# Kernel tuning notes

Measured on AMD Instinct MI355X. Metric: run time of the kernel, lower is better.

## Reference

```python
import jax, jax.numpy as jnp
import numpy as np

N, D, DC, L, K, H = 131072, 12, 4, 4, 8, 64
S = D // 2          # coupling split
B = 3.0             # spline interval [-B, B]
SLOPE = 0.2         # LeakyReLU negative slope
TOUT = (3 * K - 1) * S


def setup_inputs() -> dict:
    key = jax.random.key(0)
    ks = iter(jax.random.split(key, 40))
    def nrm(shape, scale):
        return jax.random.normal(next(ks), shape, jnp.float32) * scale
    x = jax.random.normal(next(ks), (N, D), jnp.float32)
    x_cond = jax.random.normal(next(ks), (N, DC), jnp.float32)
    rng = np.random.default_rng(0)
    convP = jnp.asarray(np.stack([np.eye(D, dtype=np.float32)[rng.permutation(D)] for _ in range(L)]))
    convS = jnp.asarray((rng.uniform(0.5, 1.5, (L, D)) * rng.choice([-1.0, 1.0], (L, D))).astype(np.float32))
    inp = {"x": x, "x_cond": x_cond, "convP": convP, "convS": convS,
           "convL": nrm((L, D, D), 0.1), "convU": nrm((L, D, D), 0.1)}
    for name, nin in (("net1", S), ("net2", S), ("nc1", DC), ("nc2", DC)):
        inp[name + "_W0"] = nrm((L, nin, H), 0.3)
        inp[name + "_b0"] = nrm((L, H), 0.05)
        inp[name + "_Wh"] = nrm((L, 2, H, H), 0.15)
        inp[name + "_bh"] = nrm((L, 2, H), 0.05)
        inp[name + "_Wl"] = nrm((L, H, TOUT), 0.15)
        inp[name + "_bl"] = nrm((L, TOUT), 0.05)
    return inp


def _leaky(h):
    return jnp.where(h >= 0, h, SLOPE * h)


def _mlp(h, W0, b0, Wh, bh, Wl, bl):
    # Linear->LeakyReLU x n_layers (LeakyReLU also after the last Linear, as in torch MLP)
    h = _leaky(h @ W0 + b0)
    for i in range(Wh.shape[0]):
        h = _leaky(h @ Wh[i] + bh[i])
    return _leaky(h @ Wl + bl)


def _spline_params(thetas):
    th = thetas.reshape(-1, S, 3 * K - 1)
    w = jax.nn.softmax(th[..., :K], axis=-1) * 2 * B
    hgt = jax.nn.softmax(th[..., K:2 * K], axis=-1) * 2 * B
    d = jax.nn.softplus(th[..., 2 * K:])
    d = jnp.pad(d, ((0, 0), (0, 0), (1, 1)), constant_values=1.0)   # [N,S,K+1]
    return w, hgt, d


def _rqs(X, widths, heights, derivs):
    # X [N,S]; widths/heights [N,S,K]; derivs [N,S,K+1]
    pad = jnp.full(X.shape + (1,), -B, X.dtype)
    # last boundary gets +1e-6 inside find_bin (in-place in torch) before search AND gathers
    bx = jnp.concatenate([pad, jnp.cumsum(widths, -1) - B], -1).at[..., -1].set(B + 1e-6)
    by = jnp.concatenate([pad, jnp.cumsum(heights, -1) - B], -1).at[..., -1].set(B)
    Xc = jnp.clip(X, -B, B)   # outside-interval values are overwritten below
    k = jnp.clip(jnp.sum(Xc[..., None] >= bx, -1) - 1, 0, K - 1)
    def g(a, idx):
        return jnp.take_along_axis(a, idx[..., None], -1)[..., 0]
    xk, xk1 = g(bx, k), g(bx, k + 1)
    yk, yk1 = g(by, k), g(by, k + 1)
    dk, dk1 = g(derivs, k), g(derivs, k + 1)
    s = (yk1 - yk) / (xk1 - xk)
    xi = (Xc - xk) / (xk1 - xk)
    den = s + (dk1 + dk - 2 * s) * xi * (1 - xi)
    Y = yk + (yk1 - yk) * (s * xi ** 2 + dk * xi * (1 - xi)) / den
    dydx = s ** 2 * (dk1 * xi ** 2 + 2 * s * xi * (1 - xi) + dk * (1 - xi) ** 2) / den ** 2
    inside = (X <= B) & (X >= -B)
    Y = jnp.where(inside, Y, X)
    ld = jnp.where(inside, jnp.log(dydx), 0.0)
    return Y, jnp.sum(ld, -1)


def reference(x, x_cond, convP, convS, convL, convU,
              net1_W0, net1_b0, net1_Wh, net1_bh, net1_Wl, net1_bl,
              net2_W0, net2_b0, net2_Wh, net2_bh, net2_Wl, net2_bl,
              nc1_W0, nc1_b0, nc1_Wh, nc1_bh, nc1_Wl, nc1_bl,
              nc2_W0, nc2_b0, nc2_Wh, nc2_bh, nc2_Wl, nc2_bl):
    logdet = jnp.zeros(x.shape[0], x.dtype)
    eye = jnp.eye(D, dtype=x.dtype)
    for l in range(L):
        # GLOW 1x1 conv (LU-parameterized)
        W = convP[l] @ (jnp.tril(convL[l], -1) + eye) @ (jnp.triu(convU[l], 1) + jnp.diag(convS[l]))
        x = x @ W
        logdet = logdet + jnp.sum(jnp.log(jnp.abs(convS[l])))
        # NSF_CL2 coupling
        first, second = x[:, S:], x[:, :S]
        t = _mlp(x_cond, nc1_W0[l], nc1_b0[l], nc1_Wh[l], nc1_bh[l], nc1_Wl[l], nc1_bl[l]) * \
            _mlp(second, net1_W0[l], net1_b0[l], net1_Wh[l], net1_bh[l], net1_Wl[l], net1_bl[l])
        w, hgt, d = _spline_params(t)
        first, ld = _rqs(first, w, hgt, d)
        logdet = logdet + ld
        t = _mlp(x_cond, nc2_W0[l], nc2_b0[l], nc2_Wh[l], nc2_bh[l], nc2_Wl[l], nc2_bl[l]) * \
            _mlp(first, net2_W0[l], net2_b0[l], net2_Wh[l], net2_bh[l], net2_Wl[l], net2_bl[l])
        w, hgt, d = _spline_params(t)
        second, ld = _rqs(second, w, hgt, d)
        logdet = logdet + ld
        x = jnp.concatenate([second, first], axis=-1)
    prior_logprob = jnp.sum(-0.5 * x ** 2 - 0.5 * float(np.log(2 * np.pi)), axis=-1)
    return (x, logdet, prior_logprob)
```

## Files before the change

### kernel.cpp

```cpp
#include <hip/hip_runtime.h>
#include <math.h>

typedef _Float16 f16;
typedef _Float16 f16x8 __attribute__((ext_vector_type(8)));
typedef __fp16 h2 __attribute__((ext_vector_type(2)));
typedef float f32x4 __attribute__((ext_vector_type(4)));
typedef unsigned int uint32;
typedef unsigned short ushort16;

#define NSAMP 131072
#define DD 12
#define LLAYERS 4
#define KK 8
#define BV 3.0f
#define BLK 256
#define NLW 17920
#define WS_WH 512
#define WS_WL 8704
#define THROW 152
#define XROW 16
#define SENTD 0.54132485f

__device__ __forceinline__ uint32 packh(float a, float b){
    union { f16 h; ushort16 u; } x, y;
    x.h = (f16)a; y.h = (f16)b;
    return (uint32)x.u | ((uint32)y.u << 16);
}
__device__ __forceinline__ float unpl(uint32 v){ union { ushort16 u; f16 h; } c; c.u = (ushort16)v; return (float)c.h; }
__device__ __forceinline__ float unph(uint32 v){ union { ushort16 u; f16 h; } c; c.u = (ushort16)(v >> 16); return (float)c.h; }

__device__ __forceinline__ h2 u2h(uint32 x){ union { uint32 u; h2 h; } c; c.u = x; return c.h; }
__device__ __forceinline__ uint32 h2u(h2 x){ union { h2 h; uint32 u; } c; c.h = x; return c.u; }
__device__ __forceinline__ h2 lk2(h2 x){
    h2 k = { (__fp16)0.2f, (__fp16)0.2f };
    return __builtin_elementwise_max(x, x * k);
}
__device__ __forceinline__ h2 pkrtz(float a, float b){ return __builtin_amdgcn_cvt_pkrtz(a, b); }
__device__ __forceinline__ float frcp(float x){ return __builtin_amdgcn_rcpf(x); }

__device__ __forceinline__ f32x4 MF(f16x8 a, f16x8 b, f32x4 c){
    return __builtin_amdgcn_mfma_f32_16x16x32_f16(a, b, c, 0, 0, 0);
}

__device__ __forceinline__ const f16x8* actRd(const f16* actW, int s, int fb){
    return (const f16x8*)((const char*)actW + s * 128 + (fb ^ ((s & 7) << 4)));
}
__device__ __forceinline__ uint2* actWr(f16* actW, int s, int fb){
    return (uint2*)((char*)actW + s * 128 + (fb ^ ((s & 7) << 4)));
}

extern "C" __global__ void nsflow_prep(
        const float* __restrict__ n1W0, const float* __restrict__ n1Wh, const float* __restrict__ n1Wl,
        const float* __restrict__ n1b0, const float* __restrict__ n1bh, const float* __restrict__ n1bl,
        const float* __restrict__ n2W0, const float* __restrict__ n2Wh, const float* __restrict__ n2Wl,
        const float* __restrict__ n2b0, const float* __restrict__ n2bh, const float* __restrict__ n2bl,
        const float* __restrict__ c1W0, const float* __restrict__ c1Wh, const float* __restrict__ c1Wl,
        const float* __restrict__ c1b0, const float* __restrict__ c1bh, const float* __restrict__ c1bl,
        const float* __restrict__ c2W0, const float* __restrict__ c2Wh, const float* __restrict__ c2Wl,
        const float* __restrict__ c2b0, const float* __restrict__ c2bh, const float* __restrict__ c2bl,
        const float* __restrict__ convP, const float* __restrict__ convS,
        const float* __restrict__ convL, const float* __restrict__ convU,
        f16* __restrict__ ws_hi, f16* __restrict__ ws_lo,
        uint32* __restrict__ wsbc, uint32* __restrict__ wsbh, float* __restrict__ wsWc){
    int NL = blockIdx.y;
    int off = blockIdx.x * 256 + threadIdx.x;
    int layer = NL >> 2, net = NL & 3;

    const float *W0, *Wh, *Wl, *b0, *bh; int nin;
    if (net == 0){ W0 = c1W0; Wh = c1Wh; Wl = c1Wl; b0 = c1b0; bh = c1bh; nin = 4; }
    else if (net == 1){ W0 = n1W0; Wh = n1Wh; Wl = n1Wl; b0 = n1b0; bh = n1bh; nin = 6; }
    else if (net == 2){ W0 = c2W0; Wh = c2Wh; Wl = c2Wl; b0 = c2b0; bh = c2bh; nin = 4; }
    else { W0 = n2W0; Wh = n2Wh; Wl = n2Wl; b0 = n2b0; bh = n2bh; nin = 6; }

    if (off < 17920){
        float w = 0.f;
        if (off < 512){
            int mt = off >> 7, r = off & 127, ln = r >> 3, j = r & 7;
            int row = mt * 16 + ln;
            if (j < nin) w = W0[(layer * nin + j) * 64 + row];
            else if (j == 7) w = b0[layer * 64 + row];
        } else if (off < 8704){
            int o = off - 512; int h = o >> 12; o &= 4095;
            int t = o >> 9, ln = (o >> 3) & 63, j = o & 7;
            int mt = t >> 1, ks = t & 1;
            int k = ks * 32 + (ln >> 4) * 8 + j, row = mt * 16 + (ln & 15);
            w = Wh[((layer * 2 + h) * 64 + k) * 64 + row];
        } else {
            int o = off - 8704;
            int t = o >> 9, ln = (o >> 3) & 63, j = o & 7;
            int mt = t >> 1, ks = t & 1;
            int k = ks * 32 + (ln >> 4) * 8 + j, m = mt * 16 + (ln & 15);
            int dd = m / 24, p = m - dd * 24;
            if (p < 23) w = Wl[(layer * 64 + k) * 138 + dd * 23 + p];
        }
        f16 hi = (f16)w;
        f16 lo = (f16)(w - (float)hi);
        ws_hi[NL * NLW + off] = hi;
        ws_lo[NL * NLW + off] = lo;
    } else if (off < 18064){
        int mm = off - 17920;
        if (net == 0 || net == 2){
            int halfI = net >> 1;
            int s = layer * 2 + halfI;
            bool isn = mm >= 72;
            int m0 = 2 * (isn ? mm - 72 : mm);
            const float* bb = isn ? (halfI ? n2bl : n1bl) : (halfI ? c2bl : c1bl);
            int dd0 = m0 / 24, p0 = m0 - dd0 * 24;
            int m1 = m0 + 1;
            int dd1 = m1 / 24, p1 = m1 - dd1 * 24;
            float v0 = (p0 < 23) ? bb[layer * 138 + dd0 * 23 + p0] : 0.f;
            float v1 = (p1 < 23) ? bb[layer * 138 + dd1 * 23 + p1] : 0.f;
            wsbc[s * 144 + mm] = packh(v0, v1);
        }
    } else if (off < 18128){
        int q = off - 18064;
        int h = q >> 5, r = q & 31, m0 = 2 * r;
        wsbh[NL * 64 + q] = packh(bh[(layer * 2 + h) * 64 + m0], bh[(layer * 2 + h) * 64 + m0 + 1]);
    } else if (off < 18705 && NL == 0){
        int idx = off - 18128;
        if (idx < 576){
            int l = idx / 144, r = idx - l * 144;
            int i = r / 12, j = r - i * 12;
            const float* P = convP + l * 144;
            const float* Lm = convL + l * 144;
            const float* Um = convU + l * 144;
            const float* Sv = convS + l * 12;
            float acc = 0.f;
            for (int a = 0; a < 12; ++a){
                float inner = 0.f;
                for (int bb2 = 0; bb2 < 12; ++bb2){
                    float m1 = (bb2 < a) ? Lm[a * 12 + bb2] : (bb2 == a ? 1.f : 0.f);
                    float m2 = (j > bb2) ? Um[bb2 * 12 + j] : (j == bb2 ? Sv[j] : 0.f);
                    inner = fmaf(m1, m2, inner);
                }
                acc = fmaf(P[i * 12 + a], inner, acc);
            }
            wsWc[idx] = acc;
        } else if (idx == 576){
            float sacc = 0.f;
            for (int q2 = 0; q2 < LLAYERS * 12; ++q2) sacc += __logf(fabsf(convS[q2]));
            wsWc[576] = sacc;
        }
    }
}

__device__ __forceinline__ void gemmL0c(const f16* __restrict__ ah, const f16* __restrict__ al,
                                        int xc0, int xc1, f16* actW, int lane){
    int l15 = lane & 15, g = lane >> 4;
    f16x8 Z = {};
    f16x8 Bf[4];
#pragma unroll
    for (int nt = 0; nt < 4; ++nt){
        union { uint4 u; f16x8 v; } cc;
        cc.u.x = (uint32)__shfl(xc0, nt * 16 + l15, 64);
        cc.u.y = (uint32)__shfl(xc1, nt * 16 + l15, 64);
        cc.u.z = 0u;
        cc.u.w = 0x3C000000u;
        Bf[nt] = cc.v;
    }
    bool g0 = (g == 0);
#pragma unroll
    for (int mt = 0; mt < 4; ++mt){
        f16x8 Ah = g0 ? *(const f16x8*)(ah + (mt * 16 + l15) * 8) : Z;
        f16x8 Al = g0 ? *(const f16x8*)(al + (mt * 16 + l15) * 8) : Z;
#pragma unroll
        for (int nt = 0; nt < 4; ++nt){
            f32x4 acc = {0.f, 0.f, 0.f, 0.f};
            acc = MF(Ah, Bf[nt], acc);
            acc = MF(Al, Bf[nt], acc);
            uint2 v = { h2u(lk2(pkrtz(acc[0], acc[1]))), h2u(lk2(pkrtz(acc[2], acc[3]))) };
            *actWr(actW, nt * 16 + l15, mt * 32 + g * 8) = v;
        }
    }
}

__device__ __forceinline__ void gemmL0n(const f16* __restrict__ ah, const f16* __restrict__ al,
                                        const f16* src, int offE,
                                        f16* actW, int lane, int widS){
    int l15 = lane & 15, g = lane >> 4;
    f16x8 Z = {};
    f16x8 Bf[4];
#pragma unroll
    for (int nt = 0; nt < 4; ++nt)
        Bf[nt] = *(const f16x8*)(src + (widS + nt * 16 + l15) * XROW + offE);
    bool g0 = (g == 0);
#pragma unroll
    for (int mt = 0; mt < 4; ++mt){
        f16x8 Ah = g0 ? *(const f16x8*)(ah + (mt * 16 + l15) * 8) : Z;
        f16x8 Al = g0 ? *(const f16x8*)(al + (mt * 16 + l15) * 8) : Z;
#pragma unroll
        for (int nt = 0; nt < 4; ++nt){
            f32x4 acc = {0.f, 0.f, 0.f, 0.f};
            acc = MF(Ah, Bf[nt], acc);
            acc = MF(Al, Bf[nt], acc);
            uint2 v = { h2u(lk2(pkrtz(acc[0], acc[1]))), h2u(lk2(pkrtz(acc[2], acc[3]))) };
            *actWr(actW, nt * 16 + l15, mt * 32 + g * 8) = v;
        }
    }
}

__device__ __forceinline__ void gemm64(const f16* __restrict__ ah,
                                       const uint32* __restrict__ bq,
                                       f16* actW, int lane){
    int l15 = lane & 15, g = lane >> 4;
    f16x8 Bf[4][2];
#pragma unroll
    for (int nt = 0; nt < 4; ++nt)
#pragma unroll
        for (int ks = 0; ks < 2; ++ks)
            Bf[nt][ks] = *actRd(actW, nt * 16 + l15, ks * 64 + g * 16);
#pragma unroll
    for (int mt = 0; mt < 4; ++mt){
        f16x8 Ah0 = *(const f16x8*)(ah + ((mt * 2 + 0) * 64 + lane) * 8);
        f16x8 Ah1 = *(const f16x8*)(ah + ((mt * 2 + 1) * 64 + lane) * 8);
        uint2 bp = *(const uint2*)(bq + mt * 8 + g * 2);
#pragma unroll
        for (int nt = 0; nt < 4; ++nt){
            f32x4 acc = {0.f, 0.f, 0.f, 0.f};
            acc = MF(Ah0, Bf[nt][0], acc);
            acc = MF(Ah1, Bf[nt][1], acc);
            uint2 v = { h2u(lk2(pkrtz(acc[0], acc[1]) + u2h(bp.x))),
                        h2u(lk2(pkrtz(acc[2], acc[3]) + u2h(bp.y))) };
            *actWr(actW, nt * 16 + l15, mt * 32 + g * 8) = v;
        }
    }
}

__device__ __forceinline__ float spline_pair(const f16* thW, f16* xst,
                                             int sbase, int halfI, int lane){
    float vsum = 0.f;
    int s32 = lane & 31;
    int hi5 = lane >> 5;
#pragma unroll 1
    for (int pass = 0; pass < 3; ++pass){
        int dd = pass * 2 + hi5;

        const f16* tr = thW + s32 * THROW + dd * 24;
        f16x8 t0 = *(const f16x8*)(tr);
        f16x8 t1 = *(const f16x8*)(tr + 8);
        f16x8 t2 = *(const f16x8*)(tr + 16);
        float th[23];
#pragma unroll
        for (int j = 0; j < 8; ++j) th[j] = (float)t0[j];
#pragma unroll
        for (int j = 0; j < 8; ++j) th[8 + j] = (float)t1[j];
#pragma unroll
        for (int j = 0; j < 7; ++j) th[16 + j] = (float)t2[j];

        float mw = th[0];
#pragma unroll
        for (int j = 1; j < KK; ++j) mw = fmaxf(mw, th[j]);
        float ew[KK]; float swsum = 0.f;
#pragma unroll
        for (int j = 0; j < KK; ++j){ ew[j] = __expf(th[j] - mw); swsum += ew[j]; }
        float iw_ = 6.0f * frcp(swsum);
        float mh = th[KK];
#pragma unroll
        for (int j = 1; j < KK; ++j) mh = fmaxf(mh, th[KK + j]);
        float eh[KK]; float shsum = 0.f;
#pragma unroll
        for (int j = 0; j < KK; ++j){ eh[j] = __expf(th[KK + j] - mh); shsum += eh[j]; }
        float ih_ = 6.0f * frcp(shsum);

        int sidx = sbase + s32;
        int slot = halfI ? dd : 8 + dd;
        float X = (float)xst[sidx * XROW + slot];
        float Xc = fminf(fmaxf(X, -BV), BV);

        float cx = -BV, cy = -BV;
        float xk = -BV, xk1 = BV, yk = -BV, yk1 = BV;
        float tl = SENTD, trh = SENTD;
#pragma unroll
        for (int j = 0; j < KK; ++j){
            float nx = (j == KK - 1) ? (BV + 1e-6f) : (cx + ew[j] * iw_);
            float ny = (j == KK - 1) ? BV : (cy + eh[j] * ih_);
            bool sel = (j == 0) || (Xc >= cx);
            if (sel){
                xk = cx; xk1 = nx; yk = cy; yk1 = ny;
                tl = (j == 0) ? SENTD : th[15 + j];
                trh = (j == KK - 1) ? SENTD : th[16 + j];
            }
            cx = nx; cy = ny;
        }
        float dk, dk1;
        {
            float z = __expf(-fabsf(tl));
            dk = fmaxf(tl, 0.f) + __logf(1.0f + z);
            float z2 = __expf(-fabsf(trh));
            dk1 = fmaxf(trh, 0.f) + __logf(1.0f + z2);
        }
        float idx_ = frcp(xk1 - xk);
        float s_ = (yk1 - yk) * idx_;
        float xi = (Xc - xk) * idx_;
        float om = 1.0f - xi;
        float xo = xi * om;
        float den = s_ + (dk1 + dk - 2.0f * s_) * xo;
        float invden = frcp(den);
        float Y = yk + (yk1 - yk) * (s_ * xi * xi + dk * xo) * invden;
        float dydx = s_ * s_ * (dk1 * xi * xi + 2.0f * s_ * xo + dk * om * om) * invden * invden;
        bool inside = (X <= BV) && (X >= -BV);
        float Yo = inside ? Y : X;
        float ldv = inside ? __logf(dydx) : 0.f;
        xst[sidx * XROW + slot] = (f16)Yo;
        vsum += ldv;
    }
    vsum += __shfl_xor(vsum, 32, 64);
    return vsum;
}

#define TAILP(NT0, NT1, BC0A, BC0B, BC1A, BC1B)                                        \
{                                                                                      \
    f16x8 Bn0a = *actRd(actW, NT0 * 16 + l15, g * 16);                                 \
    f16x8 Bn0b = *actRd(actW, NT0 * 16 + l15, 64 + g * 16);                            \
    f16x8 Bn1a = *actRd(actW, NT1 * 16 + l15, g * 16);                                 \
    f16x8 Bn1b = *actRd(actW, NT1 * 16 + l15, 64 + g * 16);                            \
    _Pragma("unroll")                                                                  \
    for (int mt = 0; mt < 9; ++mt){                                                    \
        const f16* pch = whC + WS_WL + (mt * 128 + lane) * 8;                          \
        const f16* pnh = whN + WS_WL + (mt * 128 + lane) * 8;                          \
        f16x8 AhC0 = *(const f16x8*)(pch);                                             \
        f16x8 AhC1 = *(const f16x8*)(pch + 512);                                       \
        f16x8 AhN0 = *(const f16x8*)(pnh);                                             \
        f16x8 AhN1 = *(const f16x8*)(pnh + 512);                                       \
        uint2 cq = *(const uint2*)(bcn + mt * 8 + g * 2);                              \
        uint2 nq = *(const uint2*)(bcn + 72 + mt * 8 + g * 2);                         \
        f32x4 ac = {0.f,0.f,0.f,0.f}, an = {0.f,0.f,0.f,0.f};                          \
        ac = MF(AhC0, BC0A, ac); ac = MF(AhC1, BC0B, ac);                              \
        an = MF(AhN0, Bn0a, an); an = MF(AhN1, Bn0b, an);                              \
        h2 c01 = lk2(pkrtz(ac[0], ac[1]) + u2h(cq.x));                                 \
        h2 c23 = lk2(pkrtz(ac[2], ac[3]) + u2h(cq.y));                                 \
        h2 n01 = lk2(pkrtz(an[0], an[1]) + u2h(nq.x));                                 \
        h2 n23 = lk2(pkrtz(an[2], an[3]) + u2h(nq.y));                                 \
        uint2 tv0 = { h2u(c01 * n01), h2u(c23 * n23) };                                \
        *(uint2*)(thW + l15 * THROW + mt * 16 + g4) = tv0;                             \
        f32x4 ac2 = {0.f,0.f,0.f,0.f}, an2 = {0.f,0.f,0.f,0.f};                        \
        ac2 = MF(AhC0, BC1A, ac2); ac2 = MF(AhC1, BC1B, ac2);                          \
        an2 = MF(AhN0, Bn1a, an2); an2 = MF(AhN1, Bn1b, an2);                          \
        h2 d01 = lk2(pkrtz(ac2[0], ac2[1]) + u2h(cq.x));                               \
        h2 d23 = lk2(pkrtz(ac2[2], ac2[3]) + u2h(cq.y));                               \
        h2 m01 = lk2(pkrtz(an2[0], an2[1]) + u2h(nq.x));                               \
        h2 m23 = lk2(pkrtz(an2[2], an2[3]) + u2h(nq.y));                               \
        uint2 tv1 = { h2u(d01 * m01), h2u(d23 * m23) };                                \
        *(uint2*)(thW + (16 + l15) * THROW + mt * 16 + g4) = tv1;                      \
    }                                                                                  \
    { float v = spline_pair(thW, xstS, widS + NT0 * 16, halfI, lane);                  \
      if ((lane >> 5) == (NT0 >> 1)) logdet += v; }                                    \
}

extern "C" __global__ void __launch_bounds__(BLK, 2)
nsflow_main(const float* __restrict__ x_in, const float* __restrict__ xc_in,
            const f16* __restrict__ wsh, const f16* __restrict__ wsl,
            const uint32* __restrict__ wsbc, const uint32* __restrict__ wsbh,
            const float* __restrict__ wsWc,
            float* __restrict__ out){
    __shared__ f16 xstS[256 * XROW];
    __shared__ f16 actS[4 * 64 * 64];
    __shared__ f16 thS[4 * 32 * THROW];

    int tid0 = threadIdx.x;
    int lane = tid0 & 63, wid = tid0 >> 6, widS = wid * 64;
    int l15 = lane & 15, g = lane >> 4, g4 = g * 4;
    int gsamp = blockIdx.x * BLK + tid0;

    float xr[DD];
    int xc0, xc1;
    {
        const float4* xv = (const float4*)(x_in + (size_t)gsamp * DD);
        float4 a0 = xv[0], a1 = xv[1], a2 = xv[2];
        xr[0]=a0.x; xr[1]=a0.y; xr[2]=a0.z; xr[3]=a0.w;
        xr[4]=a1.x; xr[5]=a1.y; xr[6]=a1.z; xr[7]=a1.w;
        xr[8]=a2.x; xr[9]=a2.y; xr[10]=a2.z; xr[11]=a2.w;
        float4 c0 = *(const float4*)(xc_in + (size_t)gsamp * 4);
        xc0 = (int)packh(c0.x, c0.y);
        xc1 = (int)packh(c0.z, c0.w);
    }

    float logdet = wsWc[576];
    f16* actW = actS + wid * 4096;
    f16* thW = thS + wid * (32 * THROW);

#pragma unroll 1
    for (int l = 0; l < LLAYERS; ++l){
        if (l > 0){
            uint4 r0 = *(const uint4*)(xstS + tid0 * XROW);
            uint4 r1 = *(const uint4*)(xstS + tid0 * XROW + 8);
            xr[0]=unpl(r0.x); xr[1]=unph(r0.x); xr[2]=unpl(r0.y); xr[3]=unph(r0.y);
            xr[4]=unpl(r0.z); xr[5]=unph(r0.z);
            xr[6]=unpl(r1.x); xr[7]=unph(r1.x); xr[8]=unpl(r1.y); xr[9]=unph(r1.y);
            xr[10]=unpl(r1.z); xr[11]=unph(r1.z);
        }
        float xn[DD];
#pragma unroll
        for (int j = 0; j < DD; ++j) xn[j] = 0.f;
#pragma unroll
        for (int i = 0; i < DD; ++i){
            const float4* wr = (const float4*)(wsWc + l * 144 + i * 12);
            float4 w0 = wr[0], w1 = wr[1], w2 = wr[2];
            float xi = xr[i];
            xn[0]=fmaf(xi,w0.x,xn[0]); xn[1]=fmaf(xi,w0.y,xn[1]); xn[2]=fmaf(xi,w0.z,xn[2]); xn[3]=fmaf(xi,w0.w,xn[3]);
            xn[4]=fmaf(xi,w1.x,xn[4]); xn[5]=fmaf(xi,w1.y,xn[5]); xn[6]=fmaf(xi,w1.z,xn[6]); xn[7]=fmaf(xi,w1.w,xn[7]);
            xn[8]=fmaf(xi,w2.x,xn[8]); xn[9]=fmaf(xi,w2.y,xn[9]); xn[10]=fmaf(xi,w2.z,xn[10]); xn[11]=fmaf(xi,w2.w,xn[11]);
        }
#pragma unroll
        for (int j = 0; j < DD; ++j) xr[j] = xn[j];
        {
            uint4 s0 = { packh(xr[0],xr[1]), packh(xr[2],xr[3]), packh(xr[4],xr[5]), 0x3C000000u };
            uint4 s1 = { packh(xr[6],xr[7]), packh(xr[8],xr[9]), packh(xr[10],xr[11]), 0x3C000000u };
            *(uint4*)(xstS + tid0 * XROW) = s0;
            *(uint4*)(xstS + tid0 * XROW + 8) = s1;
        }

#pragma unroll 1
        for (int halfI = 0; halfI < 2; ++halfI){
            const f16* whC = wsh + (size_t)(l * 4 + halfI * 2) * NLW;
            const f16* wlC = wsl + (size_t)(l * 4 + halfI * 2) * NLW;
            const f16* whN = whC + NLW;
            const f16* wlN = wlC + NLW;
            const uint32* bhC = wsbh + (l * 4 + halfI * 2) * 64;
            const uint32* bhN = bhC + 64;
            const uint32* bcn = wsbc + (l * 2 + halfI) * 144;

            gemmL0c(whC, wlC, xc0, xc1, actW, lane);
            gemm64(whC + WS_WH, bhC, actW, lane);
            gemm64(whC + WS_WH + 4096, bhC + 32, actW, lane);
            f16x8 Bc0a = *actRd(actW,      l15, g * 16);
            f16x8 Bc0b = *actRd(actW,      l15, 64 + g * 16);
            f16x8 Bc1a = *actRd(actW, 16 + l15, g * 16);
            f16x8 Bc1b = *actRd(actW, 16 + l15, 64 + g * 16);
            f16x8 Bc2a = *actRd(actW, 32 + l15, g * 16);
            f16x8 Bc2b = *actRd(actW, 32 + l15, 64 + g * 16);
            f16x8 Bc3a = *actRd(actW, 48 + l15, g * 16);
            f16x8 Bc3b = *actRd(actW, 48 + l15, 64 + g * 16);

            gemmL0n(whN, wlN, xstS, halfI * 8, actW, lane, widS);
            gemm64(whN + WS_WH, bhN, actW, lane);
            gemm64(whN + WS_WH + 4096, bhN + 32, actW, lane);

            TAILP(0, 1, Bc0a, Bc0b, Bc1a, Bc1b)
            TAILP(2, 3, Bc2a, Bc2b, Bc3a, Bc3b)
        }
    }

    {
        uint4 r0 = *(const uint4*)(xstS + tid0 * XROW);
        uint4 r1 = *(const uint4*)(xstS + tid0 * XROW + 8);
        xr[0]=unpl(r0.x); xr[1]=unph(r0.x); xr[2]=unpl(r0.y); xr[3]=unph(r0.y);
        xr[4]=unpl(r0.z); xr[5]=unph(r0.z);
        xr[6]=unpl(r1.x); xr[7]=unph(r1.x); xr[8]=unpl(r1.y); xr[9]=unph(r1.y);
        xr[10]=unpl(r1.z); xr[11]=unph(r1.z);
    }
    float pr = 0.f;
#pragma unroll
    for (int j = 0; j < DD; ++j) pr = fmaf(-0.5f * xr[j], xr[j], pr);
    pr -= DD * 0.91893853320467274f;

    float4* ov = (float4*)(out + (size_t)gsamp * DD);
    ov[0] = make_float4(xr[0], xr[1], xr[2], xr[3]);
    ov[1] = make_float4(xr[4], xr[5], xr[6], xr[7]);
    ov[2] = make_float4(xr[8], xr[9], xr[10], xr[11]);
    out[(size_t)NSAMP * DD + gsamp] = logdet;
    out[(size_t)NSAMP * DD + NSAMP + gsamp] = pr;
}

extern "C" void kernel_launch(void* const* d_in, const int* in_sizes, int n_in,
                              void* d_out, int out_size, void* d_ws, size_t ws_size,
                              hipStream_t stream) {
    (void)in_sizes; (void)n_in; (void)out_size; (void)ws_size;
    const float* a[30];
    for (int i = 0; i < 30; ++i) a[i] = (const float*)d_in[i];
    f16* wsh = (f16*)d_ws;
    f16* wsl = wsh + 16 * NLW;
    uint32* wsbc = (uint32*)(wsl + 16 * NLW);
    uint32* wsbh = wsbc + 8 * 144;
    float* wsWc  = (float*)(wsbh + 16 * 64);

    dim3 pg(74, 16);
    nsflow_prep<<<pg, 256, 0, stream>>>(
        a[6], a[8], a[10], a[7], a[9], a[11],
        a[12], a[14], a[16], a[13], a[15], a[17],
        a[18], a[20], a[22], a[19], a[21], a[23],
        a[24], a[26], a[28], a[25], a[27], a[29],
        a[2], a[3], a[4], a[5],
        wsh, wsl, wsbc, wsbh, wsWc);

    nsflow_main<<<NSAMP / BLK, BLK, 0, stream>>>(
        a[0], a[1], wsh, wsl, wsbc, wsbh, wsWc, (float*)d_out);
}
```

Baseline: 191.8 us.

## Shrink blocks to one wave and process spline tail in 16-sample chunks

Blocks go from four waves of 256 samples to a single 64-sample wave, with shared buffers sized per wave, and launch bounds raised to ask for three blocks per CU. The final projection and spline stage now runs in four 16-sample chunks instead of two 32-sample chunks. That shrinks the theta staging buffer and the live registers in the tail, aiming at higher occupancy. In exchange the spline loop leaves half the lanes idle on its second pass, and more small blocks must be scheduled.

```diff
diff --git a/kernel.cpp b/kernel.cpp
--- a/kernel.cpp
+++ b/kernel.cpp
@@ -13,7 +13,7 @@
 #define LLAYERS 4
 #define KK 8
 #define BV 3.0f
-#define BLK 256
+#define BLK 64
 #define NLW 17920
 #define WS_WH 512
 #define WS_WL 8704
@@ -176,13 +176,13 @@
 
 __device__ __forceinline__ void gemmL0n(const f16* __restrict__ ah, const f16* __restrict__ al,
                                         const f16* src, int offE,
-                                        f16* actW, int lane, int widS){
+                                        f16* actW, int lane){
     int l15 = lane & 15, g = lane >> 4;
     f16x8 Z = {};
     f16x8 Bf[4];
 #pragma unroll
     for (int nt = 0; nt < 4; ++nt)
-        Bf[nt] = *(const f16x8*)(src + (widS + nt * 16 + l15) * XROW + offE);
+        Bf[nt] = *(const f16x8*)(src + (nt * 16 + l15) * XROW + offE);
     bool g0 = (g == 0);
 #pragma unroll
     for (int mt = 0; mt < 4; ++mt){
@@ -226,16 +226,16 @@
     }
 }
 
-__device__ __forceinline__ float spline_pair(const f16* thW, f16* xst,
-                                             int sbase, int halfI, int lane){
+__device__ __forceinline__ float spline_chunk(const f16* thW, f16* xst,
+                                              int sbase, int halfI, int lane){
     float vsum = 0.f;
-    int s32 = lane & 31;
-    int hi5 = lane >> 5;
 #pragma unroll 1
-    for (int pass = 0; pass < 3; ++pass){
-        int dd = pass * 2 + hi5;
-
-        const f16* tr = thW + s32 * THROW + dd * 24;
+    for (int pass = 0; pass < 2; ++pass){
+        if (pass == 1 && lane >= 32) break;
+        int dd = pass * 4 + (lane >> 4);
+        int s16 = lane & 15;
+
+        const f16* tr = thW + s16 * THROW + dd * 24;
         f16x8 t0 = *(const f16x8*)(tr);
         f16x8 t1 = *(const f16x8*)(tr + 8);
         f16x8 t2 = *(const f16x8*)(tr + 16);
@@ -262,7 +262,7 @@
         for (int j = 0; j < KK; ++j){ eh[j] = __expf(th[KK + j] - mh); shsum += eh[j]; }
         float ih_ = 6.0f * frcp(shsum);
 
-        int sidx = sbase + s32;
+        int sidx = sbase + s16;
         int slot = halfI ? dd : 8 + dd;
         float X = (float)xst[sidx * XROW + slot];
         float Xc = fminf(fmaxf(X, -BV), BV);
@@ -304,16 +304,15 @@
         xst[sidx * XROW + slot] = (f16)Yo;
         vsum += ldv;
     }
+    vsum += __shfl_xor(vsum, 16, 64);
     vsum += __shfl_xor(vsum, 32, 64);
     return vsum;
 }
 
-#define TAILP(NT0, NT1, BC0A, BC0B, BC1A, BC1B)                                        \
+#define TAILP(NT, BCA, BCB)                                                            \
 {                                                                                      \
-    f16x8 Bn0a = *actRd(actW, NT0 * 16 + l15, g * 16);                                 \
-    f16x8 Bn0b = *actRd(actW, NT0 * 16 + l15, 64 + g * 16);                            \
-    f16x8 Bn1a = *actRd(actW, NT1 * 16 + l15, g * 16);                                 \
-    f16x8 Bn1b = *actRd(actW, NT1 * 16 + l15, 64 + g * 16);                            \
+    f16x8 Bna = *actRd(actW, NT * 16 + l15, g * 16);                                   \
+    f16x8 Bnb = *actRd(actW, NT * 16 + l15, 64 + g * 16);                              \
     _Pragma("unroll")                                                                  \
     for (int mt = 0; mt < 9; ++mt){                                                    \
         const f16* pch = whC + WS_WL + (mt * 128 + lane) * 8;                          \
@@ -325,42 +324,32 @@
         uint2 cq = *(const uint2*)(bcn + mt * 8 + g * 2);                              \
         uint2 nq = *(const uint2*)(bcn + 72 + mt * 8 + g * 2);                         \
         f32x4 ac = {0.f,0.f,0.f,0.f}, an = {0.f,0.f,0.f,0.f};                          \
-        ac = MF(AhC0, BC0A, ac); ac = MF(AhC1, BC0B, ac);                              \
-        an = MF(AhN0, Bn0a, an); an = MF(AhN1, Bn0b, an);                              \
+        ac = MF(AhC0, BCA, ac); ac = MF(AhC1, BCB, ac);                                \
+        an = MF(AhN0, Bna, an); an = MF(AhN1, Bnb, an);                                \
         h2 c01 = lk2(pkrtz(ac[0], ac[1]) + u2h(cq.x));                                 \
         h2 c23 = lk2(pkrtz(ac[2], ac[3]) + u2h(cq.y));                                 \
         h2 n01 = lk2(pkrtz(an[0], an[1]) + u2h(nq.x));                                 \
         h2 n23 = lk2(pkrtz(an[2], an[3]) + u2h(nq.y));                                 \
         uint2 tv0 = { h2u(c01 * n01), h2u(c23 * n23) };                                \
         *(uint2*)(thW + l15 * THROW + mt * 16 + g4) = tv0;                             \
-        f32x4 ac2 = {0.f,0.f,0.f,0.f}, an2 = {0.f,0.f,0.f,0.f};                        \
-        ac2 = MF(AhC0, BC1A, ac2); ac2 = MF(AhC1, BC1B, ac2);                          \
-        an2 = MF(AhN0, Bn1a, an2); an2 = MF(AhN1, Bn1b, an2);                          \
-        h2 d01 = lk2(pkrtz(ac2[0], ac2[1]) + u2h(cq.x));                               \
-        h2 d23 = lk2(pkrtz(ac2[2], ac2[3]) + u2h(cq.y));                               \
-        h2 m01 = lk2(pkrtz(an2[0], an2[1]) + u2h(nq.x));                               \
-        h2 m23 = lk2(pkrtz(an2[2], an2[3]) + u2h(nq.y));                               \
-        uint2 tv1 = { h2u(d01 * m01), h2u(d23 * m23) };                                \
-        *(uint2*)(thW + (16 + l15) * THROW + mt * 16 + g4) = tv1;                      \
     }                                                                                  \
-    { float v = spline_pair(thW, xstS, widS + NT0 * 16, halfI, lane);                  \
-      if ((lane >> 5) == (NT0 >> 1)) logdet += v; }                                    \
-}
-
-extern "C" __global__ void __launch_bounds__(BLK, 2)
+    { float v = spline_chunk(thW, xstS, NT * 16, halfI, lane);                         \
+      if (g == NT) logdet += v; }                                                      \
+}
+
+extern "C" __global__ void __launch_bounds__(BLK, 3)
 nsflow_main(const float* __restrict__ x_in, const float* __restrict__ xc_in,
             const f16* __restrict__ wsh, const f16* __restrict__ wsl,
             const uint32* __restrict__ wsbc, const uint32* __restrict__ wsbh,
             const float* __restrict__ wsWc,
             float* __restrict__ out){
-    __shared__ f16 xstS[256 * XROW];
-    __shared__ f16 actS[4 * 64 * 64];
-    __shared__ f16 thS[4 * 32 * THROW];
-
-    int tid0 = threadIdx.x;
-    int lane = tid0 & 63, wid = tid0 >> 6, widS = wid * 64;
+    __shared__ f16 xstS[BLK * XROW];
+    __shared__ f16 actS[64 * 64];
+    __shared__ f16 thS[16 * THROW];
+
+    int lane = threadIdx.x & 63;
     int l15 = lane & 15, g = lane >> 4, g4 = g * 4;
-    int gsamp = blockIdx.x * BLK + tid0;
+    int gsamp = blockIdx.x * BLK + lane;
 
     float xr[DD];
     int xc0, xc1;
@@ -376,14 +365,14 @@
     }
 
     float logdet = wsWc[576];
-    f16* actW = actS + wid * 4096;
-    f16* thW = thS + wid * (32 * THROW);
+    f16* actW = actS;
+    f16* thW = thS;
 
 #pragma unroll 1
     for (int l = 0; l < LLAYERS; ++l){
         if (l > 0){
-            uint4 r0 = *(const uint4*)(xstS + tid0 * XROW);
-            uint4 r1 = *(const uint4*)(xstS + tid0 * XROW + 8);
+            uint4 r0 = *(const uint4*)(xstS + lane * XROW);
+            uint4 r1 = *(const uint4*)(xstS + lane * XROW + 8);
             xr[0]=unpl(r0.x); xr[1]=unph(r0.x); xr[2]=unpl(r0.y); xr[3]=unph(r0.y);
             xr[4]=unpl(r0.z); xr[5]=unph(r0.z);
             xr[6]=unpl(r1.x); xr[7]=unph(r1.x); xr[8]=unpl(r1.y); xr[9]=unph(r1.y);
@@ -406,8 +395,8 @@
         {
             uint4 s0 = { packh(xr[0],xr[1]), packh(xr[2],xr[3]), packh(xr[4],xr[5]), 0x3C000000u };
             uint4 s1 = { packh(xr[6],xr[7]), packh(xr[8],xr[9]), packh(xr[10],xr[11]), 0x3C000000u };
-            *(uint4*)(xstS + tid0 * XROW) = s0;
-            *(uint4*)(xstS + tid0 * XROW + 8) = s1;
+            *(uint4*)(xstS + lane * XROW) = s0;
+            *(uint4*)(xstS + lane * XROW + 8) = s1;
         }
 
 #pragma unroll 1
@@ -432,18 +421,20 @@
             f16x8 Bc3a = *actRd(actW, 48 + l15, g * 16);
             f16x8 Bc3b = *actRd(actW, 48 + l15, 64 + g * 16);
 
-            gemmL0n(whN, wlN, xstS, halfI * 8, actW, lane, widS);
+            gemmL0n(whN, wlN, xstS, halfI * 8, actW, lane);
             gemm64(whN + WS_WH, bhN, actW, lane);
             gemm64(whN + WS_WH + 4096, bhN + 32, actW, lane);
 
-            TAILP(0, 1, Bc0a, Bc0b, Bc1a, Bc1b)
-            TAILP(2, 3, Bc2a, Bc2b, Bc3a, Bc3b)
+            TAILP(0, Bc0a, Bc0b)
+            TAILP(1, Bc1a, Bc1b)
+            TAILP(2, Bc2a, Bc2b)
+            TAILP(3, Bc3a, Bc3b)
         }
     }
 
     {
-        uint4 r0 = *(const uint4*)(xstS + tid0 * XROW);
-        uint4 r1 = *(const uint4*)(xstS + tid0 * XROW + 8);
+        uint4 r0 = *(const uint4*)(xstS + lane * XROW);
+        uint4 r1 = *(const uint4*)(xstS + lane * XROW + 8);
         xr[0]=unpl(r0.x); xr[1]=unph(r0.x); xr[2]=unpl(r0.y); xr[3]=unph(r0.y);
         xr[4]=unpl(r0.z); xr[5]=unph(r0.z);
         xr[6]=unpl(r1.x); xr[7]=unph(r1.x); xr[8]=unpl(r1.y); xr[9]=unph(r1.y);
```

Result: slower. 297.0 us (+54.8%).

## Drop low-half fp16 split in first-layer GEMMs and fold log2e into spline logits

Applied to the files above, without the earlier changes.

Removes the hi/lo fp16 error-compensation MFMA and its weight load from the first MLP layer of both the conditioning and main nets, so that layer uses a single fp16 MFMA. Pre-scales the main-net final-layer weights and biases for the width and height logits by log2(e), which lets the softmax use exp2 instead of exp. Also rewrites the max reductions as a flatter tree. This trims MFMA work, loads and transcendental overhead, at the cost of reduced first-layer precision. The log2e fold relies on the product with the conditioning net, which is scaled only on the main-net side.

```diff
diff --git a/kernel.cpp b/kernel.cpp
--- a/kernel.cpp
+++ b/kernel.cpp
@@ -20,6 +20,7 @@
 #define THROW 152
 #define XROW 16
 #define SENTD 0.54132485f
+#define LOG2E 1.44269504f
 
 __device__ __forceinline__ uint32 packh(float a, float b){
     union { f16 h; ushort16 u; } x, y;
@@ -91,7 +92,10 @@
             int mt = t >> 1, ks = t & 1;
             int k = ks * 32 + (ln >> 4) * 8 + j, m = mt * 16 + (ln & 15);
             int dd = m / 24, p = m - dd * 24;
-            if (p < 23) w = Wl[(layer * 64 + k) * 138 + dd * 23 + p];
+            if (p < 23){
+                w = Wl[(layer * 64 + k) * 138 + dd * 23 + p];
+                if ((net == 1 || net == 3) && p < 16) w *= LOG2E;
+            }
         }
         f16 hi = (f16)w;
         f16 lo = (f16)(w - (float)hi);
@@ -110,6 +114,8 @@
             int dd1 = m1 / 24, p1 = m1 - dd1 * 24;
             float v0 = (p0 < 23) ? bb[layer * 138 + dd0 * 23 + p0] : 0.f;
             float v1 = (p1 < 23) ? bb[layer * 138 + dd1 * 23 + p1] : 0.f;
+            if (isn && p0 < 16) v0 *= LOG2E;
+            if (isn && p1 < 16) v1 *= LOG2E;
             wsbc[s * 144 + mm] = packh(v0, v1);
         }
     } else if (off < 18128){
@@ -144,7 +150,7 @@
     }
 }
 
-__device__ __forceinline__ void gemmL0c(const f16* __restrict__ ah, const f16* __restrict__ al,
+__device__ __forceinline__ void gemmL0c(const f16* __restrict__ ah,
                                         int xc0, int xc1, f16* actW, int lane){
     int l15 = lane & 15, g = lane >> 4;
     f16x8 Z = {};
@@ -162,19 +168,17 @@
 #pragma unroll
     for (int mt = 0; mt < 4; ++mt){
         f16x8 Ah = g0 ? *(const f16x8*)(ah + (mt * 16 + l15) * 8) : Z;
-        f16x8 Al = g0 ? *(const f16x8*)(al + (mt * 16 + l15) * 8) : Z;
 #pragma unroll
         for (int nt = 0; nt < 4; ++nt){
             f32x4 acc = {0.f, 0.f, 0.f, 0.f};
             acc = MF(Ah, Bf[nt], acc);
-            acc = MF(Al, Bf[nt], acc);
             uint2 v = { h2u(lk2(pkrtz(acc[0], acc[1]))), h2u(lk2(pkrtz(acc[2], acc[3]))) };
             *actWr(actW, nt * 16 + l15, mt * 32 + g * 8) = v;
         }
     }
 }
 
-__device__ __forceinline__ void gemmL0n(const f16* __restrict__ ah, const f16* __restrict__ al,
+__device__ __forceinline__ void gemmL0n(const f16* __restrict__ ah,
                                         const f16* src, int offE,
                                         f16* actW, int lane, int widS){
     int l15 = lane & 15, g = lane >> 4;
@@ -187,12 +191,10 @@
 #pragma unroll
     for (int mt = 0; mt < 4; ++mt){
         f16x8 Ah = g0 ? *(const f16x8*)(ah + (mt * 16 + l15) * 8) : Z;
-        f16x8 Al = g0 ? *(const f16x8*)(al + (mt * 16 + l15) * 8) : Z;
 #pragma unroll
         for (int nt = 0; nt < 4; ++nt){
             f32x4 acc = {0.f, 0.f, 0.f, 0.f};
             acc = MF(Ah, Bf[nt], acc);
-            acc = MF(Al, Bf[nt], acc);
             uint2 v = { h2u(lk2(pkrtz(acc[0], acc[1]))), h2u(lk2(pkrtz(acc[2], acc[3]))) };
             *actWr(actW, nt * 16 + l15, mt * 32 + g * 8) = v;
         }
@@ -247,19 +249,21 @@
 #pragma unroll
         for (int j = 0; j < 7; ++j) th[16 + j] = (float)t2[j];
 
-        float mw = th[0];
-#pragma unroll
-        for (int j = 1; j < KK; ++j) mw = fmaxf(mw, th[j]);
+        float mw = fmaxf(fmaxf(th[0], th[1]), th[2]);
+        mw = fmaxf(fmaxf(mw, th[3]), th[4]);
+        mw = fmaxf(fmaxf(mw, th[5]), th[6]);
+        mw = fmaxf(mw, th[7]);
         float ew[KK]; float swsum = 0.f;
 #pragma unroll
-        for (int j = 0; j < KK; ++j){ ew[j] = __expf(th[j] - mw); swsum += ew[j]; }
+        for (int j = 0; j < KK; ++j){ ew[j] = exp2f(th[j] - mw); swsum += ew[j]; }
         float iw_ = 6.0f * frcp(swsum);
-        float mh = th[KK];
-#pragma unroll
-        for (int j = 1; j < KK; ++j) mh = fmaxf(mh, th[KK + j]);
+        float mh = fmaxf(fmaxf(th[8], th[9]), th[10]);
+        mh = fmaxf(fmaxf(mh, th[11]), th[12]);
+        mh = fmaxf(fmaxf(mh, th[13]), th[14]);
+        mh = fmaxf(mh, th[15]);
         float eh[KK]; float shsum = 0.f;
 #pragma unroll
-        for (int j = 0; j < KK; ++j){ eh[j] = __expf(th[KK + j] - mh); shsum += eh[j]; }
+        for (int j = 0; j < KK; ++j){ eh[j] = exp2f(th[KK + j] - mh); shsum += eh[j]; }
         float ih_ = 6.0f * frcp(shsum);
 
         int sidx = sbase + s32;
@@ -349,7 +353,7 @@
 
 extern "C" __global__ void __launch_bounds__(BLK, 2)
 nsflow_main(const float* __restrict__ x_in, const float* __restrict__ xc_in,
-            const f16* __restrict__ wsh, const f16* __restrict__ wsl,
+            const f16* __restrict__ wsh,
             const uint32* __restrict__ wsbc, const uint32* __restrict__ wsbh,
             const float* __restrict__ wsWc,
             float* __restrict__ out){
@@ -413,14 +417,12 @@
 #pragma unroll 1
         for (int halfI = 0; halfI < 2; ++halfI){
             const f16* whC = wsh + (size_t)(l * 4 + halfI * 2) * NLW;
-            const f16* wlC = wsl + (size_t)(l * 4 + halfI * 2) * NLW;
             const f16* whN = whC + NLW;
-            const f16* wlN = wlC + NLW;
             const uint32* bhC = wsbh + (l * 4 + halfI * 2) * 64;
             const uint32* bhN = bhC + 64;
             const uint32* bcn = wsbc + (l * 2 + halfI) * 144;
 
-            gemmL0c(whC, wlC, xc0, xc1, actW, lane);
+            gemmL0c(whC, xc0, xc1, actW, lane);
             gemm64(whC + WS_WH, bhC, actW, lane);
             gemm64(whC + WS_WH + 4096, bhC + 32, actW, lane);
             f16x8 Bc0a = *actRd(actW,      l15, g * 16);
@@ -432,7 +434,7 @@
             f16x8 Bc3a = *actRd(actW, 48 + l15, g * 16);
             f16x8 Bc3b = *actRd(actW, 48 + l15, 64 + g * 16);
 
-            gemmL0n(whN, wlN, xstS, halfI * 8, actW, lane, widS);
+            gemmL0n(whN, xstS, halfI * 8, actW, lane, widS);
             gemm64(whN + WS_WH, bhN, actW, lane);
             gemm64(whN + WS_WH + 4096, bhN + 32, actW, lane);
 
@@ -484,5 +486,5 @@
         wsh, wsl, wsbc, wsbh, wsWc);
 
     nsflow_main<<<NSAMP / BLK, BLK, 0, stream>>>(
-        a[0], a[1], wsh, wsl, wsbc, wsbh, wsWc, (float*)d_out);
-}
+        a[0], a[1], wsh, wsbc, wsbh, wsWc, (float*)d_out);
+}
```

Result: slower. 196.2 us (+2.3%).
